# Performance work log

Hardware: AMD Instinct MI355X
Metric: run time of the kernel (lower is better)

Reference implementation:

```python
import jax, jax.numpy as jnp
import numpy as np

B, S, D = 8, 160, 256


def setup_inputs() -> dict:
    key = jax.random.key(0)
    kx, kw, kb = jax.random.split(key, 3)
    x = jax.random.normal(kx, (B, S, D), dtype=jnp.float32)
    # torch nn.Linear(2D, D): weight [D, 2D], bias [D]; store transposed W [2D, D]
    lim = 1.0 / np.sqrt(2 * D)
    W = jax.random.uniform(kw, (2 * D, D), minval=-lim, maxval=lim, dtype=jnp.float32)
    b = jax.random.uniform(kb, (D,), minval=-lim, maxval=lim, dtype=jnp.float32)
    return {"x": x, "W": W, "b": b}


def reference(x, W, b):
    Bsz, Ssz, Dsz = x.shape
    # all i<j pairs in the same order as the nested python loop (i outer, j inner)
    idx_i, idx_j = jnp.triu_indices(Ssz, k=1)  # each [P], P = S(S-1)/2
    # fc_rel(cat(x_i, x_j)) = x_i @ W[:D] + x_j @ W[D:] + b
    Wi, Wj = W[:Dsz], W[Dsz:]
    xa = jnp.einsum('bsd,de->bse', x, Wi)  # [B,S,D]
    xb = jnp.einsum('bsd,de->bse', x, Wj)  # [B,S,D]
    return xa[:, idx_i, :] + xb[:, idx_j, :] + b  # [B,P,D]
```

## Files before the change

kernel.cpp:

```cpp
#include <hip/hip_runtime.h>

#define SS 160
#define DD 256
#define BB 8
#define NPAIR 12720
#define M_TOT (BB * SS)
#define TOTROWS (BB * NPAIR)
#define NWAVES 8192

__global__ __launch_bounds__(256) void gemm_kernel(const float* __restrict__ x,
                                                   const float* __restrict__ W,
                                                   const float* __restrict__ bias,
                                                   float* __restrict__ y) {
    const int BM = 32, BN = 64, BK = 32;
    __shared__ float As[BK][BM + 1];
    __shared__ float Bs[BK][BN];

    const int n0 = blockIdx.x * BN;
    const int m0 = blockIdx.y * BM;
    const int half = (n0 >= DD) ? 1 : 0;
    const float* Wbase = W + (half ? DD * DD : 0);
    const int ncol0 = n0 - (half ? DD : 0);

    const int tid = threadIdx.x;
    const int tx = tid & 15;
    const int ty = tid >> 4;

    const int ar = tid >> 3;
    const int ac = (tid & 7) << 2;
    const int bkr = tid >> 4;
    const int bnc = (tid & 15) << 2;

    float acc0[4] = {0.f, 0.f, 0.f, 0.f};
    float acc1[4] = {0.f, 0.f, 0.f, 0.f};

    for (int k0 = 0; k0 < DD; k0 += BK) {
        float4 av = *(const float4*)(x + (m0 + ar) * DD + k0 + ac);
        float4 b0 = *(const float4*)(Wbase + (k0 + bkr) * DD + ncol0 + bnc);
        float4 b1 = *(const float4*)(Wbase + (k0 + bkr + 16) * DD + ncol0 + bnc);
        __syncthreads();
        As[ac + 0][ar] = av.x;
        As[ac + 1][ar] = av.y;
        As[ac + 2][ar] = av.z;
        As[ac + 3][ar] = av.w;
        *(float4*)(&Bs[bkr][bnc])      = b0;
        *(float4*)(&Bs[bkr + 16][bnc]) = b1;
        __syncthreads();
#pragma unroll
        for (int kk = 0; kk < BK; ++kk) {
            float a0 = As[kk][ty];
            float a1 = As[kk][ty + 16];
            float4 bv = *(const float4*)(&Bs[kk][tx << 2]);
            acc0[0] += a0 * bv.x; acc0[1] += a0 * bv.y;
            acc0[2] += a0 * bv.z; acc0[3] += a0 * bv.w;
            acc1[0] += a1 * bv.x; acc1[1] += a1 * bv.y;
            acc1[2] += a1 * bv.z; acc1[3] += a1 * bv.w;
        }
    }

    float4 bias4 = make_float4(0.f, 0.f, 0.f, 0.f);
    if (!half) bias4 = *(const float4*)(bias + ncol0 + (tx << 2));

    float* yout = y + (half ? M_TOT * DD : 0);
    float4 r0, r1;
    r0.x = acc0[0] + bias4.x; r0.y = acc0[1] + bias4.y;
    r0.z = acc0[2] + bias4.z; r0.w = acc0[3] + bias4.w;
    r1.x = acc1[0] + bias4.x; r1.y = acc1[1] + bias4.y;
    r1.z = acc1[2] + bias4.z; r1.w = acc1[3] + bias4.w;
    *(float4*)(yout + (m0 + ty) * DD + ncol0 + (tx << 2))      = r0;
    *(float4*)(yout + (m0 + ty + 16) * DD + ncol0 + (tx << 2)) = r1;
}

__global__ __launch_bounds__(256) void expand_kernel(const float* __restrict__ y,
                                                     float* __restrict__ out) {
    const int gw   = (blockIdx.x << 2) + (threadIdx.x >> 6);
    const int lane = threadIdx.x & 63;

    int r0 = (int)(((long long)gw * TOTROWS) / NWAVES);
    int r1 = (int)(((long long)(gw + 1) * TOTROWS) / NWAVES);

    int b = (unsigned)r0 / NPAIR;
    int p = r0 - b * NPAIR;

    float disc = sqrtf((float)(101761 - 8 * p));
    int i = (int)((319.0f - disc) * 0.5f);
    if (i < 0) i = 0;
    if (i > SS - 2) i = SS - 2;
    while (i > 0 && (i * (2 * SS - 1 - i)) / 2 > p) --i;
    while (((i + 1) * (2 * SS - 2 - i)) / 2 <= p) ++i;
    int j = i + 1 + p - (i * (2 * SS - 1 - i)) / 2;

    const float4* ya4 = (const float4*)y;
    const float4* yb4 = (const float4*)(y + M_TOT * DD);

    float4 va = ya4[((b * SS + i) << 6) + lane];
    const float4* pb = yb4 + ((b * SS + j) << 6) + lane;
    float4* po = (float4*)out + ((long long)r0 << 6) + lane;

    for (int r = r0; r < r1; ++r) {
        float4 vb = *pb;
        float4 o;
        o.x = va.x + vb.x; o.y = va.y + vb.y;
        o.z = va.z + vb.z; o.w = va.w + vb.w;
        *po = o;
        po += 64;
        ++j;
        pb += 64;
        if (j == SS) {
            ++i;
            if (i == SS - 1) { ++b; i = 0; }
            j = i + 1;
            if (r + 1 < r1) {
                va = ya4[((b * SS + i) << 6) + lane];
                pb = yb4 + ((b * SS + j) << 6) + lane;
            }
        }
    }
}

extern "C" void kernel_launch(void* const* d_in, const int* in_sizes, int n_in,
                              void* d_out, int out_size, void* d_ws, size_t ws_size,
                              hipStream_t stream) {
    const float* x    = (const float*)d_in[0];
    const float* W    = (const float*)d_in[1];
    const float* bias = (const float*)d_in[2];
    float* y   = (float*)d_ws;
    float* out = (float*)d_out;

    dim3 gemm_grid(512 / 64, 1280 / 32);
    gemm_kernel<<<gemm_grid, 256, 0, stream>>>(x, W, bias, y);

    expand_kernel<<<NWAVES / 4, 256, 0, stream>>>(y, out);
}
```

Measured before the change: 128.0 us.

## Use nontemporal stores and run-based inner loop in expand; widen GEMM block

The expand kernel now walks each contiguous run of j for a fixed i in a tight unrolled loop and writes output with nontemporal stores, so the 104 MB write stream does not pollute the cache. The GEMM moves to 512 threads with BK=64, and each thread computes one output row instead of two. The expand output is bandwidth-bound, so the nontemporal store hint is the main lever. The GEMM change adds threads but lowers work per thread.

```diff
diff --git a/kernel.cpp b/kernel.cpp
--- a/kernel.cpp
+++ b/kernel.cpp
@@ -8,11 +8,13 @@
 #define TOTROWS (BB * NPAIR)
 #define NWAVES 8192
 
-__global__ __launch_bounds__(256) void gemm_kernel(const float* __restrict__ x,
+typedef float vfloat4 __attribute__((ext_vector_type(4)));
+
+__global__ __launch_bounds__(512) void gemm_kernel(const float* __restrict__ x,
                                                    const float* __restrict__ W,
                                                    const float* __restrict__ bias,
                                                    float* __restrict__ y) {
-    const int BM = 32, BN = 64, BK = 32;
+    const int BM = 32, BN = 64, BK = 64;
     __shared__ float As[BK][BM + 1];
     __shared__ float Bs[BK][BN];
 
@@ -26,35 +28,31 @@
     const int tx = tid & 15;
     const int ty = tid >> 4;
 
-    const int ar = tid >> 3;
-    const int ac = (tid & 7) << 2;
+    const int ar = tid >> 4;
+    const int ac = (tid & 15) << 2;
     const int bkr = tid >> 4;
     const int bnc = (tid & 15) << 2;
 
-    float acc0[4] = {0.f, 0.f, 0.f, 0.f};
-    float acc1[4] = {0.f, 0.f, 0.f, 0.f};
+    float acc[4] = {0.f, 0.f, 0.f, 0.f};
 
     for (int k0 = 0; k0 < DD; k0 += BK) {
         float4 av = *(const float4*)(x + (m0 + ar) * DD + k0 + ac);
         float4 b0 = *(const float4*)(Wbase + (k0 + bkr) * DD + ncol0 + bnc);
-        float4 b1 = *(const float4*)(Wbase + (k0 + bkr + 16) * DD + ncol0 + bnc);
+        float4 b1 = *(const float4*)(Wbase + (k0 + bkr + 32) * DD + ncol0 + bnc);
         __syncthreads();
         As[ac + 0][ar] = av.x;
         As[ac + 1][ar] = av.y;
         As[ac + 2][ar] = av.z;
         As[ac + 3][ar] = av.w;
         *(float4*)(&Bs[bkr][bnc])      = b0;
-        *(float4*)(&Bs[bkr + 16][bnc]) = b1;
+        *(float4*)(&Bs[bkr + 32][bnc]) = b1;
         __syncthreads();
 #pragma unroll
         for (int kk = 0; kk < BK; ++kk) {
-            float a0 = As[kk][ty];
-            float a1 = As[kk][ty + 16];
+            float a = As[kk][ty];
             float4 bv = *(const float4*)(&Bs[kk][tx << 2]);
-            acc0[0] += a0 * bv.x; acc0[1] += a0 * bv.y;
-            acc0[2] += a0 * bv.z; acc0[3] += a0 * bv.w;
-            acc1[0] += a1 * bv.x; acc1[1] += a1 * bv.y;
-            acc1[2] += a1 * bv.z; acc1[3] += a1 * bv.w;
+            acc[0] += a * bv.x; acc[1] += a * bv.y;
+            acc[2] += a * bv.z; acc[3] += a * bv.w;
         }
     }
 
@@ -62,13 +60,10 @@
     if (!half) bias4 = *(const float4*)(bias + ncol0 + (tx << 2));
 
     float* yout = y + (half ? M_TOT * DD : 0);
-    float4 r0, r1;
-    r0.x = acc0[0] + bias4.x; r0.y = acc0[1] + bias4.y;
-    r0.z = acc0[2] + bias4.z; r0.w = acc0[3] + bias4.w;
-    r1.x = acc1[0] + bias4.x; r1.y = acc1[1] + bias4.y;
-    r1.z = acc1[2] + bias4.z; r1.w = acc1[3] + bias4.w;
-    *(float4*)(yout + (m0 + ty) * DD + ncol0 + (tx << 2))      = r0;
-    *(float4*)(yout + (m0 + ty + 16) * DD + ncol0 + (tx << 2)) = r1;
+    float4 r;
+    r.x = acc[0] + bias4.x; r.y = acc[1] + bias4.y;
+    r.z = acc[2] + bias4.z; r.w = acc[3] + bias4.w;
+    *(float4*)(yout + (m0 + ty) * DD + ncol0 + (tx << 2)) = r;
 }
 
 __global__ __launch_bounds__(256) void expand_kernel(const float* __restrict__ y,
@@ -90,31 +85,27 @@
     while (((i + 1) * (2 * SS - 2 - i)) / 2 <= p) ++i;
     int j = i + 1 + p - (i * (2 * SS - 1 - i)) / 2;
 
-    const float4* ya4 = (const float4*)y;
-    const float4* yb4 = (const float4*)(y + M_TOT * DD);
+    const vfloat4* __restrict__ ya4 = (const vfloat4*)y;
+    const vfloat4* __restrict__ yb4 = (const vfloat4*)(y + M_TOT * DD);
+    vfloat4* po = (vfloat4*)out + ((long long)r0 << 6) + lane;
 
-    float4 va = ya4[((b * SS + i) << 6) + lane];
-    const float4* pb = yb4 + ((b * SS + j) << 6) + lane;
-    float4* po = (float4*)out + ((long long)r0 << 6) + lane;
-
-    for (int r = r0; r < r1; ++r) {
-        float4 vb = *pb;
-        float4 o;
-        o.x = va.x + vb.x; o.y = va.y + vb.y;
-        o.z = va.z + vb.z; o.w = va.w + vb.w;
-        *po = o;
-        po += 64;
-        ++j;
-        pb += 64;
-        if (j == SS) {
-            ++i;
-            if (i == SS - 1) { ++b; i = 0; }
-            j = i + 1;
-            if (r + 1 < r1) {
-                va = ya4[((b * SS + i) << 6) + lane];
-                pb = yb4 + ((b * SS + j) << 6) + lane;
-            }
+    int r = r0;
+    while (r < r1) {
+        vfloat4 va = ya4[((b * SS + i) << 6) + lane];
+        const vfloat4* pb = yb4 + ((b * SS + j) << 6) + lane;
+        int run = SS - j;
+        if (run > r1 - r) run = r1 - r;
+#pragma unroll 2
+        for (int t = 0; t < run; ++t) {
+            vfloat4 vb = pb[t * 64];
+            vfloat4 o = va + vb;
+            __builtin_nontemporal_store(o, po);
+            po += 64;
         }
+        r += run;
+        ++i;
+        if (i == SS - 1) { ++b; i = 0; }
+        j = i + 1;
     }
 }
 
@@ -128,7 +119,7 @@
     float* out = (float*)d_out;
 
     dim3 gemm_grid(512 / 64, 1280 / 32);
-    gemm_kernel<<<gemm_grid, 256, 0, stream>>>(x, W, bias, y);
+    gemm_kernel<<<gemm_grid, 512, 0, stream>>>(x, W, bias, y);
 
     expand_kernel<<<NWAVES / 4, 256, 0, stream>>>(y, out);
 }
```

Result: slower. 133.9 us (+4.6%).
